# Kernel optimization log

Hardware: AMD Instinct MI355X
Metric: run time of the kernel (lower is better)

The kernel has to match this reference:

```python
import jax, jax.numpy as jnp
import numpy as np
from jax import lax

B, Hm, Wm = 8, 128, 128          # batch, mesh height, mesh width
DIM, HEADS, DH, G, K = 128, 8, 64, 64, 3
INNER = HEADS * DH
N = Hm * Wm


def setup_inputs() -> dict:
    key = jax.random.key(0)
    ks = jax.random.split(key, 12)
    s = 0.02
    x = jax.random.normal(ks[0], (B, N, DIM), dtype=jnp.float32)
    conv_fx_w = jax.random.normal(ks[1], (K, K, DIM, INNER), dtype=jnp.float32) * s
    conv_fx_b = jnp.zeros((INNER,), dtype=jnp.float32)
    conv_x_w = jax.random.normal(ks[2], (K, K, DIM, INNER), dtype=jnp.float32) * s
    conv_x_b = jnp.zeros((INNER,), dtype=jnp.float32)
    # nn.Linear(dim_head, slice_num): weight (G, DH), orthogonal-init approximated by scaled normal
    slice_w = jax.random.normal(ks[3], (G, DH), dtype=jnp.float32) * (1.0 / np.sqrt(DH))
    slice_b = jnp.zeros((G,), dtype=jnp.float32)
    temperature = jnp.ones((1, HEADS, 1, 1), dtype=jnp.float32) * 0.5
    wq = jax.random.normal(ks[4], (DH, DH), dtype=jnp.float32) * s
    wk = jax.random.normal(ks[5], (DH, DH), dtype=jnp.float32) * s
    wv = jax.random.normal(ks[6], (DH, DH), dtype=jnp.float32) * s
    out_w = jax.random.normal(ks[7], (DIM, INNER), dtype=jnp.float32) * s
    out_b = jnp.zeros((DIM,), dtype=jnp.float32)
    return {
        "x": x,
        "conv_fx_w": conv_fx_w, "conv_fx_b": conv_fx_b,
        "conv_x_w": conv_x_w, "conv_x_b": conv_x_b,
        "slice_w": slice_w, "slice_b": slice_b,
        "temperature": temperature,
        "wq": wq, "wk": wk, "wv": wv,
        "out_w": out_w, "out_b": out_b,
    }


def _conv(z, w, b):
    # z: (B, H, W, Cin); w: (K, K, Cin, Cout); SAME padding, stride 1
    return lax.conv_general_dilated(
        z, w, window_strides=(1, 1), padding="SAME",
        dimension_numbers=("NHWC", "HWIO", "NHWC")) + b


def reference(x, conv_fx_w, conv_fx_b, conv_x_w, conv_x_b,
              slice_w, slice_b, temperature, wq, wk, wv, out_w, out_b):
    b, n, c = x.shape
    xi = x.reshape(b, Hm, Wm, c)
    # (B,H,W,INNER) -> (B,N,heads,dh) -> (B,heads,N,dh)
    fx_mid = _conv(xi, conv_fx_w, conv_fx_b).reshape(b, n, HEADS, DH).transpose(0, 2, 1, 3)
    x_mid = _conv(xi, conv_x_w, conv_x_b).reshape(b, n, HEADS, DH).transpose(0, 2, 1, 3)

    temp = jnp.clip(temperature, 0.1, 5.0)  # (1,heads,1,1)
    logits = (jnp.einsum("bhnc,gc->bhng", x_mid, slice_w) + slice_b) / temp
    slice_weights = jax.nn.softmax(logits, axis=-1)         # (B,heads,N,G)

    slice_norm = slice_weights.sum(axis=2)                   # (B,heads,G)
    slice_token = jnp.einsum("bhnc,bhng->bhgc", fx_mid, slice_weights)
    slice_token = slice_token / (slice_norm + 1e-5)[..., None]

    q = jnp.einsum("bhgc,dc->bhgd", slice_token, wq)
    k = jnp.einsum("bhgc,dc->bhgd", slice_token, wk)
    v = jnp.einsum("bhgc,dc->bhgd", slice_token, wv)

    scale = DH ** (-0.5)
    attn = jax.nn.softmax(jnp.einsum("bhgd,bhkd->bhgk", q, k) * scale, axis=-1)
    out_slice = jnp.einsum("bhgk,bhkd->bhgd", attn, v)       # (B,heads,G,dh)

    out_x = jnp.einsum("bhgc,bhng->bhnc", out_slice, slice_weights)
    out_x = out_x.transpose(0, 2, 1, 3).reshape(b, n, INNER)
    return jnp.einsum("bnc,dc->bnd", out_x, out_w) + out_b
```

## Files before the change

### kernel.cpp

```cpp
#include <hip/hip_runtime.h>
#include <stdint.h>

#define BATCH 8
#define HEADS 8
#define HM 128
#define WM 128
#define NPIX (HM*WM)
#define DIMC 128
#define DH 64
#define GS 64
#define INNER 512
#define KTOT 1152
#define XT_LD 128
#define PT_LD 128

typedef unsigned short u16;
typedef short v8s __attribute__((ext_vector_type(8)));
typedef float v4f __attribute__((ext_vector_type(4)));

__device__ __forceinline__ u16 f2bf(float f) {
    unsigned x = __float_as_uint(f);
    return (u16)((x + 0x7fffu + ((x >> 16) & 1u)) >> 16);
}
__device__ __forceinline__ float bf2f(u16 u) { return __uint_as_float(((unsigned)u) << 16); }
__device__ __forceinline__ unsigned cvtpk(float lo, float hi) {
    unsigned r;
    asm("v_cvt_pk_bf16_f32 %0, %1, %2" : "=v"(r) : "v"(lo), "v"(hi));
    return r;
}

union BF8 { uint4 v; u16 s[8]; };

__global__ __launch_bounds__(256) void k_build_w(
    const float* __restrict__ wx, const float* __restrict__ wfx,
    const float* __restrict__ slw, const float* __restrict__ temp,
    u16* __restrict__ wcatT, u16* __restrict__ wfxT)
{
    __shared__ float sw_l[GS][DH + 1];
    __shared__ float wx_l[INNER];
    int row = blockIdx.x;
    int t = threadIdx.x;
    for (int i = t; i < GS * DH; i += 256) sw_l[i >> 6][i & 63] = slw[i];
    for (int i = t; i < INNER; i += 256) wx_l[i] = wx[(size_t)row * INNER + i];
    __syncthreads();
#pragma unroll
    for (int j = 0; j < 2; j++) {
        int co = j * 256 + t;
        int h = co >> 6, g = co & 63;
        float s = 0.f;
        for (int c = 0; c < DH; c++) s = fmaf(wx_l[h * 64 + c], sw_l[g][c], s);
        float tv = fminf(fmaxf(temp[h], 0.1f), 5.0f);
        wcatT[(size_t)co * KTOT + row] = f2bf(s / tv);
        wfxT[(size_t)co * KTOT + row] = f2bf(wfx[(size_t)row * INNER + co]);
    }
}

__global__ __launch_bounds__(512) void k_build_b(
    const float* __restrict__ bx, const float* __restrict__ slw,
    const float* __restrict__ slb, const float* __restrict__ temp,
    float* __restrict__ bcatL)
{
    int co = threadIdx.x;
    int h = co >> 6, g = co & 63;
    float s = slb[g];
    for (int c = 0; c < DH; c++) s = fmaf(bx[h * 64 + c], slw[g * 64 + c], s);
    float tv = fminf(fmaxf(temp[h], 0.1f), 5.0f);
    bcatL[co] = s / tv;
}

union SmemC {
    u16 X[130 * XT_LD];
    struct { u16 SwT[128][PT_LD]; u16 FxT[128][PT_LD]; } e;
};

__global__ __launch_bounds__(256) void k_conv2(
    const float* __restrict__ xin, const u16* __restrict__ wcatT,
    const u16* __restrict__ wfxT, const float* __restrict__ bcatL,
    const float* __restrict__ bfx, u16* __restrict__ swbT,
    float* __restrict__ straw, float* __restrict__ norm)
{
    __shared__ SmemC sm;
    int pt = blockIdx.x;
    int b = pt >> 7, y = pt & 127;
    int ct = blockIdx.y;
    int cob = ct << 7;
    int t = threadIdx.x;
    int lane = t & 63, wave = t >> 6;
    int wr = wave >> 1, wc = wave & 1;
    int l16 = lane & 15, lk = lane >> 4;

    v4f accL[4][4], accF[4][4];
#pragma unroll
    for (int i = 0; i < 4; i++)
#pragma unroll
        for (int j = 0; j < 4; j++) {
            accL[i][j] = v4f{0.f, 0.f, 0.f, 0.f};
            accF[i][j] = v4f{0.f, 0.f, 0.f, 0.f};
        }

    const u16* wlb[4]; const u16* wfb[4];
#pragma unroll
    for (int nj = 0; nj < 4; nj++) {
        size_t roff = (size_t)(cob + wc * 64 + nj * 16 + l16) * KTOT + lk * 8;
        wlb[nj] = wcatT + roff;
        wfb[nj] = wfxT + roff;
    }

    v8s bL[2][4], bF[2][4];
    {
#pragma unroll
        for (int nj = 0; nj < 4; nj++) {
            bL[0][nj] = *(const v8s*)(wlb[nj]);
            bF[0][nj] = *(const v8s*)(wfb[nj]);
        }
    }

    for (int ky = 0; ky < 3; ky++) {
        int yy = y + ky - 1;
        bool yok = (unsigned)yy < (unsigned)HM;
        const float* xrow = xin + ((size_t)b * NPIX + (size_t)yy * WM) * DIMC;
        if (ky) __syncthreads();
        for (int i = t; i < 2080; i += 256) {
            int row = i >> 4, k8 = i & 15;
            int px = row - 1;
            uint4 o;
            if (yok && (unsigned)px < (unsigned)WM) {
                const float4* p = (const float4*)(xrow + (size_t)px * DIMC + k8 * 8);
                float4 fa = p[0], fb = p[1];
                o = make_uint4(cvtpk(fa.x, fa.y), cvtpk(fa.z, fa.w),
                               cvtpk(fb.x, fb.y), cvtpk(fb.z, fb.w));
            } else {
                o = make_uint4(0u, 0u, 0u, 0u);
            }
            *(uint4*)(sm.X + row * XT_LD + ((k8 ^ (row & 7)) * 8)) = o;
        }
        __syncthreads();
#pragma unroll
        for (int cc = 0; cc < 12; cc++) {
            int g = ky * 12 + cc;
            if (g < 35) {
                int wo = ((g + 1) >> 2) * 128 + ((g + 1) & 3) * 32;
#pragma unroll
                for (int nj = 0; nj < 4; nj++) {
                    bL[(cc + 1) & 1][nj] = *(const v8s*)(wlb[nj] + wo);
                    bF[(cc + 1) & 1][nj] = *(const v8s*)(wfb[nj] + wo);
                }
            }
            int kx = cc >> 2, c4 = cc & 3;
            int xr7 = (l16 + kx) & 7;
            const u16* xb = sm.X + (wr * 64 + l16 + kx) * XT_LD;
            int xo = (((c4 * 4 + lk) ^ xr7) * 8);
            v8s av[4];
#pragma unroll
            for (int mi = 0; mi < 4; mi++)
                av[mi] = *(const v8s*)(xb + mi * 16 * XT_LD + xo);
#pragma unroll
            for (int mi = 0; mi < 4; mi++)
#pragma unroll
                for (int nj = 0; nj < 4; nj++) {
                    accL[mi][nj] = __builtin_amdgcn_mfma_f32_16x16x32_bf16(
                        av[mi], bL[cc & 1][nj], accL[mi][nj], 0, 0, 0);
                    accF[mi][nj] = __builtin_amdgcn_mfma_f32_16x16x32_bf16(
                        av[mi], bF[cc & 1][nj], accF[mi][nj], 0, 0, 0);
                }
        }
    }
    __syncthreads();

    float bbL[4], bbF[4];
#pragma unroll
    for (int nj = 0; nj < 4; nj++) {
        bbL[nj] = bcatL[cob + wc * 64 + nj * 16 + l16];
        bbF[nj] = bfx[cob + wc * 64 + nj * 16 + l16];
    }

#pragma unroll
    for (int mi = 0; mi < 4; mi++) {
#pragma unroll
        for (int q = 0; q < 4; q++) {
            float m = accL[mi][0][q] + bbL[0];
#pragma unroll
            for (int nj = 1; nj < 4; nj++) m = fmaxf(m, accL[mi][nj][q] + bbL[nj]);
            m = fmaxf(m, __shfl_xor(m, 1));
            m = fmaxf(m, __shfl_xor(m, 2));
            m = fmaxf(m, __shfl_xor(m, 4));
            m = fmaxf(m, __shfl_xor(m, 8));
            float ssum = 0.f;
#pragma unroll
            for (int nj = 0; nj < 4; nj++) {
                float e = __expf(accL[mi][nj][q] + bbL[nj] - m);
                accL[mi][nj][q] = e; ssum += e;
            }
            ssum += __shfl_xor(ssum, 1);
            ssum += __shfl_xor(ssum, 2);
            ssum += __shfl_xor(ssum, 4);
            ssum += __shfl_xor(ssum, 8);
            float inv = 1.f / ssum;
#pragma unroll
            for (int nj = 0; nj < 4; nj++) accL[mi][nj][q] *= inv;
        }
    }

#pragma unroll
    for (int nj = 0; nj < 4; nj++) {
        float pn = 0.f;
#pragma unroll
        for (int mi = 0; mi < 4; mi++)
#pragma unroll
            for (int q = 0; q < 4; q++) pn += accL[mi][nj][q];
        pn += __shfl_xor(pn, 16);
        pn += __shfl_xor(pn, 32);
        if (lk == 0)
            atomicAdd(&norm[(size_t)(b * HEADS + 2 * ct + wc) * GS + nj * 16 + l16], pn);
    }

#pragma unroll
    for (int nj = 0; nj < 4; nj++) {
        int grow = wc * 64 + nj * 16 + l16;
        int r7 = l16 & 7;
#pragma unroll
        for (int mi = 0; mi < 4; mi++) {
            int off = (((wr * 8 + mi * 2 + (lk >> 1)) ^ r7) * 8) + (lk & 1) * 4;
            uint2 wv;
            wv.x = cvtpk(accL[mi][nj][0], accL[mi][nj][1]);
            wv.y = cvtpk(accL[mi][nj][2], accL[mi][nj][3]);
            *(uint2*)&sm.e.SwT[grow][off] = wv;
            uint2 fv;
            fv.x = cvtpk(accF[mi][nj][0] + bbF[nj], accF[mi][nj][1] + bbF[nj]);
            fv.y = cvtpk(accF[mi][nj][2] + bbF[nj], accF[mi][nj][3] + bbF[nj]);
            *(uint2*)&sm.e.FxT[grow][off] = fv;
        }
    }
    __syncthreads();

    v4f pacc[2][4];
#pragma unroll
    for (int i = 0; i < 2; i++)
#pragma unroll
        for (int j = 0; j < 4; j++) pacc[i][j] = v4f{0.f, 0.f, 0.f, 0.f};
    {
        int r7 = l16 & 7;
#pragma unroll
        for (int c = 0; c < 4; c++) {
            int ko = (((c * 4 + lk) ^ r7) * 8);
            v8s aw[2], bw[4];
#pragma unroll
            for (int mi = 0; mi < 2; mi++)
                aw[mi] = *(const v8s*)(&sm.e.SwT[wc * 64 + wr * 32 + mi * 16 + l16][0] + ko);
#pragma unroll
            for (int nj = 0; nj < 4; nj++)
                bw[nj] = *(const v8s*)(&sm.e.FxT[wc * 64 + nj * 16 + l16][0] + ko);
#pragma unroll
            for (int mi = 0; mi < 2; mi++)
#pragma unroll
                for (int nj = 0; nj < 4; nj++)
                    pacc[mi][nj] = __builtin_amdgcn_mfma_f32_16x16x32_bf16(
                        aw[mi], bw[nj], pacc[mi][nj], 0, 0, 0);
        }
    }

#pragma unroll
    for (int it = 0; it < 8; it++) {
        int chunk = it * 256 + t;
        int g = chunk >> 4;
        int p8 = chunk & 15;
        uint4 v = *(const uint4*)(&sm.e.SwT[g][0] + ((p8 ^ (g & 7)) * 8));
        size_t di = (((size_t)(b * HEADS + 2 * ct + (g >> 6)) * GS + (g & 63)) * NPIX)
                    + (size_t)y * WM + p8 * 8;
        *(uint4*)&swbT[di] = v;
    }

    int bh = b * HEADS + 2 * ct + wc;
#pragma unroll
    for (int mi = 0; mi < 2; mi++)
#pragma unroll
        for (int nj = 0; nj < 4; nj++)
#pragma unroll
            for (int q = 0; q < 4; q++) {
                int g = wr * 32 + mi * 16 + lk * 4 + q;
                int dh = nj * 16 + l16;
                atomicAdd(&straw[((size_t)bh * GS + g) * DH + dh], pacc[mi][nj][q]);
            }
}

__global__ __launch_bounds__(256) void k_attn(
    const float* __restrict__ straw, const float* __restrict__ norm,
    const float* __restrict__ wq, const float* __restrict__ wk, const float* __restrict__ wv,
    const float* __restrict__ outw, float* __restrict__ m1)
{
    __shared__ float lds[4][64][64];
    int bh = blockIdx.x, h = bh & 7;
    int t = threadIdx.x;
    for (int i = t; i < 4096; i += 256) {
        int g = i >> 6;
        lds[0][g][i & 63] = straw[(size_t)bh * 4096 + i] / (norm[bh * 64 + g] + 1e-5f);
    }
    __syncthreads();
    int g = t >> 2, d0 = (t & 3) << 4;
    for (int d = d0; d < d0 + 16; d++) {
        float sq = 0.f, sk = 0.f, sv = 0.f;
        for (int c = 0; c < 64; c++) {
            float sc = lds[0][g][c];
            sq = fmaf(sc, wq[d * 64 + c], sq);
            sk = fmaf(sc, wk[d * 64 + c], sk);
            sv = fmaf(sc, wv[d * 64 + c], sv);
        }
        lds[1][g][d] = sq; lds[2][g][d] = sk; lds[3][g][d] = sv;
    }
    __syncthreads();
    float attnrow[16];
    for (int k2 = d0, i = 0; k2 < d0 + 16; k2++, i++) {
        float s = 0.f;
        for (int d = 0; d < 64; d++) s = fmaf(lds[1][g][d], lds[2][k2][d], s);
        attnrow[i] = s * 0.125f;
    }
    __syncthreads();
    for (int i = 0; i < 16; i++) lds[0][g][d0 + i] = attnrow[i];
    __syncthreads();
    if (t < 64) {
        float mx = -1e30f;
        for (int j = 0; j < 64; j++) mx = fmaxf(mx, lds[0][t][j]);
        float s = 0.f;
        for (int j = 0; j < 64; j++) { float e = __expf(lds[0][t][j] - mx); lds[0][t][j] = e; s += e; }
        float inv = 1.f / s;
        for (int j = 0; j < 64; j++) lds[0][t][j] *= inv;
    }
    __syncthreads();
    float osrow[16];
    for (int d = d0, i = 0; d < d0 + 16; d++, i++) {
        float s = 0.f;
        for (int kx = 0; kx < 64; kx++) s = fmaf(lds[0][g][kx], lds[3][kx][d], s);
        osrow[i] = s;
    }
    __syncthreads();
    for (int i = 0; i < 16; i++) lds[2][g][d0 + i] = osrow[i];
    __syncthreads();
    int dimb = (t & 3) << 5;
    for (int dim = dimb; dim < dimb + 32; dim++) {
        float s = 0.f;
        for (int c = 0; c < 64; c++)
            s = fmaf(lds[2][g][c], outw[(size_t)dim * INNER + h * 64 + c], s);
        m1[((size_t)bh * 64 + g) * DIMC + dim] = s;
    }
}

__global__ __launch_bounds__(256) void k_final(
    const u16* __restrict__ swbT, const float* __restrict__ m1,
    const float* __restrict__ outb, float* __restrict__ out)
{
    __shared__ float As[32][68];
    __shared__ float Bs[32][128];
    int b = blockIdx.x, nt = blockIdx.y;
    int t = threadIdx.x;
    int tn = t & 15, tm = t >> 4;
    float acc[4][8];
#pragma unroll
    for (int i = 0; i < 4; i++)
#pragma unroll
        for (int j = 0; j < 8; j++) acc[i][j] = 0.f;
    int n0 = nt * 64;
    int gg = t >> 3, nq = (t & 7) * 8;
    int g2 = t >> 3, dd = (t & 7) * 16;
    for (int h = 0; h < HEADS; h++) {
        const u16* swp = swbT + (size_t)(b * HEADS + h) * GS * NPIX;
        const float* m1p = m1 + (size_t)(b * HEADS + h) * GS * DIMC;
        for (int g0 = 0; g0 < 64; g0 += 32) {
            __syncthreads();
            BF8 av8; av8.v = *(const uint4*)&swp[(size_t)(g0 + gg) * NPIX + n0 + nq];
#pragma unroll
            for (int i = 0; i < 8; i++) As[gg][nq + i] = bf2f(av8.s[i]);
            const float* bp = m1p + (size_t)(g0 + g2) * DIMC + dd;
            *(float4*)&Bs[g2][dd + 0]  = *(const float4*)(bp + 0);
            *(float4*)&Bs[g2][dd + 4]  = *(const float4*)(bp + 4);
            *(float4*)&Bs[g2][dd + 8]  = *(const float4*)(bp + 8);
            *(float4*)&Bs[g2][dd + 12] = *(const float4*)(bp + 12);
            __syncthreads();
#pragma unroll
            for (int kk = 0; kk < 32; kk++) {
                float4 a = *(const float4*)&As[kk][tm * 4];
                float4 b0 = *(const float4*)&Bs[kk][tn * 4];
                float4 b1 = *(const float4*)&Bs[kk][tn * 4 + 64];
                float av[4] = {a.x, a.y, a.z, a.w};
                float bv[8] = {b0.x, b0.y, b0.z, b0.w, b1.x, b1.y, b1.z, b1.w};
#pragma unroll
                for (int i = 0; i < 4; i++)
#pragma unroll
                    for (int j = 0; j < 8; j++)
                        acc[i][j] = fmaf(av[i], bv[j], acc[i][j]);
            }
        }
    }
    float4 bias0 = *(const float4*)&outb[tn * 4];
    float4 bias1 = *(const float4*)&outb[64 + tn * 4];
#pragma unroll
    for (int i = 0; i < 4; i++) {
        size_t n = (size_t)n0 + tm * 4 + i;
        size_t rb = ((size_t)b * NPIX + n) * DIMC;
        float4 r0, r1;
        r0.x = acc[i][0] + bias0.x; r0.y = acc[i][1] + bias0.y;
        r0.z = acc[i][2] + bias0.z; r0.w = acc[i][3] + bias0.w;
        r1.x = acc[i][4] + bias1.x; r1.y = acc[i][5] + bias1.y;
        r1.z = acc[i][6] + bias1.z; r1.w = acc[i][7] + bias1.w;
        *(float4*)&out[rb + tn * 4] = r0;
        *(float4*)&out[rb + 64 + tn * 4] = r1;
    }
}

extern "C" void kernel_launch(void* const* d_in, const int* in_sizes, int n_in,
                              void* d_out, int out_size, void* d_ws, size_t ws_size,
                              hipStream_t stream)
{
    (void)in_sizes; (void)n_in; (void)out_size;
    const float* x    = (const float*)d_in[0];
    const float* wfx  = (const float*)d_in[1];
    const float* bfx  = (const float*)d_in[2];
    const float* wx   = (const float*)d_in[3];
    const float* bx   = (const float*)d_in[4];
    const float* slw  = (const float*)d_in[5];
    const float* slb  = (const float*)d_in[6];
    const float* temp = (const float*)d_in[7];
    const float* wq   = (const float*)d_in[8];
    const float* wk   = (const float*)d_in[9];
    const float* wv   = (const float*)d_in[10];
    const float* outw = (const float*)d_in[11];
    const float* outb = (const float*)d_in[12];
    float* out = (float*)d_out;
    float* W = (float*)d_ws;

    u16*   wcatT = (u16*)W;
    u16*   wfxT  = (u16*)(W + 294912);
    float* bcatL = W + 589824;
    float* norm  = W + 590336;
    float* straw = W + 594432;
    float* m1    = W + 856576;
    u16*   swbT  = (u16*)(W + 1380864);
    const size_t need = 1380864ull * 4 + 67108864ull * 2;
    if (ws_size < need) return;

    hipMemsetAsync(norm, 0, (4096 + 262144) * sizeof(float), stream);

    k_build_w<<<dim3(1152), 256, 0, stream>>>(wx, wfx, slw, temp, wcatT, wfxT);
    k_build_b<<<dim3(1), 512, 0, stream>>>(bx, slw, slb, temp, bcatL);
    k_conv2<<<dim3(1024, 4), 256, 0, stream>>>(x, wcatT, wfxT, bcatL, bfx, swbT, straw, norm);
    k_attn<<<dim3(64), 256, 0, stream>>>(straw, norm, wq, wk, wv, outw, m1);
    k_final<<<dim3(8, 256), 256, 0, stream>>>(swbT, m1, outb, out);
}
```

Before: 1.312 ms.

## Widen conv block to 256 output channels with 512 threads to reuse input tile

The fused conv kernel now computes 256 output channels (four heads) per block using 8 waves instead of 128 channels with 4 waves. The staged bf16 input row tile is loaded once per block, so half as many blocks each redo the fp32 load and conversion of the input rows. The epilogue (slice-token MFMA, swbT store, atomics) is processed in two head-pair passes through the same shared buffer, which adds extra barriers. The 512-thread blocks with large accumulator arrays may cut occupancy and raise register pressure.

```diff
diff --git a/kernel.cpp b/kernel.cpp
--- a/kernel.cpp
+++ b/kernel.cpp
@@ -73,7 +73,7 @@
     struct { u16 SwT[128][PT_LD]; u16 FxT[128][PT_LD]; } e;
 };
 
-__global__ __launch_bounds__(256) void k_conv2(
+__global__ __launch_bounds__(512) void k_conv2(
     const float* __restrict__ xin, const u16* __restrict__ wcatT,
     const u16* __restrict__ wfxT, const float* __restrict__ bcatL,
     const float* __restrict__ bfx, u16* __restrict__ swbT,
@@ -83,11 +83,12 @@
     int pt = blockIdx.x;
     int b = pt >> 7, y = pt & 127;
     int ct = blockIdx.y;
-    int cob = ct << 7;
+    int cob = ct << 8;
     int t = threadIdx.x;
     int lane = t & 63, wave = t >> 6;
-    int wr = wave >> 1, wc = wave & 1;
+    int w_half = wave >> 2, w_co = wave & 3;
     int l16 = lane & 15, lk = lane >> 4;
+    int hb = b * HEADS + 4 * ct;
 
     v4f accL[4][4], accF[4][4];
 #pragma unroll
@@ -101,38 +102,41 @@
     const u16* wlb[4]; const u16* wfb[4];
 #pragma unroll
     for (int nj = 0; nj < 4; nj++) {
-        size_t roff = (size_t)(cob + wc * 64 + nj * 16 + l16) * KTOT + lk * 8;
+        size_t roff = (size_t)(cob + w_co * 64 + nj * 16 + l16) * KTOT + lk * 8;
         wlb[nj] = wcatT + roff;
         wfb[nj] = wfxT + roff;
     }
 
     v8s bL[2][4], bF[2][4];
-    {
-#pragma unroll
-        for (int nj = 0; nj < 4; nj++) {
-            bL[0][nj] = *(const v8s*)(wlb[nj]);
-            bF[0][nj] = *(const v8s*)(wfb[nj]);
-        }
-    }
-
+#pragma unroll
+    for (int nj = 0; nj < 4; nj++) {
+        bL[0][nj] = *(const v8s*)(wlb[nj]);
+        bF[0][nj] = *(const v8s*)(wfb[nj]);
+    }
+
+#pragma unroll
     for (int ky = 0; ky < 3; ky++) {
         int yy = y + ky - 1;
         bool yok = (unsigned)yy < (unsigned)HM;
         const float* xrow = xin + ((size_t)b * NPIX + (size_t)yy * WM) * DIMC;
         if (ky) __syncthreads();
-        for (int i = t; i < 2080; i += 256) {
-            int row = i >> 4, k8 = i & 15;
-            int px = row - 1;
-            uint4 o;
-            if (yok && (unsigned)px < (unsigned)WM) {
-                const float4* p = (const float4*)(xrow + (size_t)px * DIMC + k8 * 8);
-                float4 fa = p[0], fb = p[1];
-                o = make_uint4(cvtpk(fa.x, fa.y), cvtpk(fa.z, fa.w),
-                               cvtpk(fb.x, fb.y), cvtpk(fb.z, fb.w));
-            } else {
-                o = make_uint4(0u, 0u, 0u, 0u);
-            }
-            *(uint4*)(sm.X + row * XT_LD + ((k8 ^ (row & 7)) * 8)) = o;
+#pragma unroll
+        for (int it = 0; it < 5; it++) {
+            int i = t + it * 512;
+            if (i < 2080) {
+                int row = i >> 4, k8 = i & 15;
+                int px = row - 1;
+                uint4 o;
+                if (yok && (unsigned)px < (unsigned)WM) {
+                    const float4* p = (const float4*)(xrow + (size_t)px * DIMC + k8 * 8);
+                    float4 fa = p[0], fb = p[1];
+                    o = make_uint4(cvtpk(fa.x, fa.y), cvtpk(fa.z, fa.w),
+                                   cvtpk(fb.x, fb.y), cvtpk(fb.z, fb.w));
+                } else {
+                    o = make_uint4(0u, 0u, 0u, 0u);
+                }
+                *(uint4*)(sm.X + row * XT_LD + ((k8 ^ (row & 7)) * 8)) = o;
+            }
         }
         __syncthreads();
 #pragma unroll
@@ -148,7 +152,7 @@
             }
             int kx = cc >> 2, c4 = cc & 3;
             int xr7 = (l16 + kx) & 7;
-            const u16* xb = sm.X + (wr * 64 + l16 + kx) * XT_LD;
+            const u16* xb = sm.X + (w_half * 64 + l16 + kx) * XT_LD;
             int xo = (((c4 * 4 + lk) ^ xr7) * 8);
             v8s av[4];
 #pragma unroll
@@ -170,8 +174,8 @@
     float bbL[4], bbF[4];
 #pragma unroll
     for (int nj = 0; nj < 4; nj++) {
-        bbL[nj] = bcatL[cob + wc * 64 + nj * 16 + l16];
-        bbF[nj] = bfx[cob + wc * 64 + nj * 16 + l16];
+        bbL[nj] = bcatL[cob + w_co * 64 + nj * 16 + l16];
+        bbF[nj] = bfx[cob + w_co * 64 + nj * 16 + l16];
     }
 
 #pragma unroll
@@ -211,76 +215,82 @@
         pn += __shfl_xor(pn, 16);
         pn += __shfl_xor(pn, 32);
         if (lk == 0)
-            atomicAdd(&norm[(size_t)(b * HEADS + 2 * ct + wc) * GS + nj * 16 + l16], pn);
-    }
-
-#pragma unroll
-    for (int nj = 0; nj < 4; nj++) {
-        int grow = wc * 64 + nj * 16 + l16;
-        int r7 = l16 & 7;
-#pragma unroll
-        for (int mi = 0; mi < 4; mi++) {
-            int off = (((wr * 8 + mi * 2 + (lk >> 1)) ^ r7) * 8) + (lk & 1) * 4;
-            uint2 wv;
-            wv.x = cvtpk(accL[mi][nj][0], accL[mi][nj][1]);
-            wv.y = cvtpk(accL[mi][nj][2], accL[mi][nj][3]);
-            *(uint2*)&sm.e.SwT[grow][off] = wv;
-            uint2 fv;
-            fv.x = cvtpk(accF[mi][nj][0] + bbF[nj], accF[mi][nj][1] + bbF[nj]);
-            fv.y = cvtpk(accF[mi][nj][2] + bbF[nj], accF[mi][nj][3] + bbF[nj]);
-            *(uint2*)&sm.e.FxT[grow][off] = fv;
-        }
-    }
-    __syncthreads();
-
-    v4f pacc[2][4];
-#pragma unroll
-    for (int i = 0; i < 2; i++)
-#pragma unroll
-        for (int j = 0; j < 4; j++) pacc[i][j] = v4f{0.f, 0.f, 0.f, 0.f};
-    {
-        int r7 = l16 & 7;
-#pragma unroll
-        for (int c = 0; c < 4; c++) {
-            int ko = (((c * 4 + lk) ^ r7) * 8);
-            v8s aw[2], bw[4];
+            atomicAdd(&norm[(size_t)(hb + w_co) * GS + nj * 16 + l16], pn);
+    }
+
+#pragma unroll
+    for (int hp = 0; hp < 2; hp++) {
+        bool mine = ((w_co >> 1) == hp);
+        if (mine) {
+            int wcp = w_co & 1;
+#pragma unroll
+            for (int nj = 0; nj < 4; nj++) {
+                int grow = wcp * 64 + nj * 16 + l16;
+                int r7 = l16 & 7;
+#pragma unroll
+                for (int mi = 0; mi < 4; mi++) {
+                    int off = (((w_half * 8 + mi * 2 + (lk >> 1)) ^ r7) * 8) + (lk & 1) * 4;
+                    uint2 wv;
+                    wv.x = cvtpk(accL[mi][nj][0], accL[mi][nj][1]);
+                    wv.y = cvtpk(accL[mi][nj][2], accL[mi][nj][3]);
+                    *(uint2*)&sm.e.SwT[grow][off] = wv;
+                    uint2 fv;
+                    fv.x = cvtpk(accF[mi][nj][0] + bbF[nj], accF[mi][nj][1] + bbF[nj]);
+                    fv.y = cvtpk(accF[mi][nj][2] + bbF[nj], accF[mi][nj][3] + bbF[nj]);
+                    *(uint2*)&sm.e.FxT[grow][off] = fv;
+                }
+            }
+        }
+        __syncthreads();
+        if (mine) {
+            int wcp = w_co & 1;
+            v4f pacc[2][4];
+#pragma unroll
+            for (int i = 0; i < 2; i++)
+#pragma unroll
+                for (int j = 0; j < 4; j++) pacc[i][j] = v4f{0.f, 0.f, 0.f, 0.f};
+            int r7 = l16 & 7;
+#pragma unroll
+            for (int c = 0; c < 4; c++) {
+                int ko = (((c * 4 + lk) ^ r7) * 8);
+                v8s aw[2], bw[4];
+#pragma unroll
+                for (int mi = 0; mi < 2; mi++)
+                    aw[mi] = *(const v8s*)(&sm.e.SwT[wcp * 64 + w_half * 32 + mi * 16 + l16][0] + ko);
+#pragma unroll
+                for (int nj = 0; nj < 4; nj++)
+                    bw[nj] = *(const v8s*)(&sm.e.FxT[wcp * 64 + nj * 16 + l16][0] + ko);
+#pragma unroll
+                for (int mi = 0; mi < 2; mi++)
+#pragma unroll
+                    for (int nj = 0; nj < 4; nj++)
+                        pacc[mi][nj] = __builtin_amdgcn_mfma_f32_16x16x32_bf16(
+                            aw[mi], bw[nj], pacc[mi][nj], 0, 0, 0);
+            }
+            int bh2 = hb + 2 * hp + wcp;
 #pragma unroll
             for (int mi = 0; mi < 2; mi++)
-                aw[mi] = *(const v8s*)(&sm.e.SwT[wc * 64 + wr * 32 + mi * 16 + l16][0] + ko);
-#pragma unroll
-            for (int nj = 0; nj < 4; nj++)
-                bw[nj] = *(const v8s*)(&sm.e.FxT[wc * 64 + nj * 16 + l16][0] + ko);
-#pragma unroll
-            for (int mi = 0; mi < 2; mi++)
 #pragma unroll
                 for (int nj = 0; nj < 4; nj++)
-                    pacc[mi][nj] = __builtin_amdgcn_mfma_f32_16x16x32_bf16(
-                        aw[mi], bw[nj], pacc[mi][nj], 0, 0, 0);
-        }
-    }
-
-#pragma unroll
-    for (int it = 0; it < 8; it++) {
-        int chunk = it * 256 + t;
-        int g = chunk >> 4;
-        int p8 = chunk & 15;
-        uint4 v = *(const uint4*)(&sm.e.SwT[g][0] + ((p8 ^ (g & 7)) * 8));
-        size_t di = (((size_t)(b * HEADS + 2 * ct + (g >> 6)) * GS + (g & 63)) * NPIX)
-                    + (size_t)y * WM + p8 * 8;
-        *(uint4*)&swbT[di] = v;
-    }
-
-    int bh = b * HEADS + 2 * ct + wc;
-#pragma unroll
-    for (int mi = 0; mi < 2; mi++)
-#pragma unroll
-        for (int nj = 0; nj < 4; nj++)
-#pragma unroll
-            for (int q = 0; q < 4; q++) {
-                int g = wr * 32 + mi * 16 + lk * 4 + q;
-                int dh = nj * 16 + l16;
-                atomicAdd(&straw[((size_t)bh * GS + g) * DH + dh], pacc[mi][nj][q]);
-            }
+#pragma unroll
+                    for (int q = 0; q < 4; q++) {
+                        int g = w_half * 32 + mi * 16 + lk * 4 + q;
+                        int dh = nj * 16 + l16;
+                        atomicAdd(&straw[((size_t)bh2 * GS + g) * DH + dh], pacc[mi][nj][q]);
+                    }
+        }
+#pragma unroll
+        for (int it = 0; it < 4; it++) {
+            int chunk = it * 512 + t;
+            int gi = chunk >> 4;
+            int p8 = chunk & 15;
+            uint4 v = *(const uint4*)(&sm.e.SwT[gi][0] + ((p8 ^ (gi & 7)) * 8));
+            size_t di = (((size_t)(hb + 2 * hp + (gi >> 6)) * GS + (gi & 63)) * NPIX)
+                        + (size_t)y * WM + p8 * 8;
+            *(uint4*)&swbT[di] = v;
+        }
+        __syncthreads();
+    }
 }
 
 __global__ __launch_bounds__(256) void k_attn(
@@ -441,7 +451,7 @@
 
     k_build_w<<<dim3(1152), 256, 0, stream>>>(wx, wfx, slw, temp, wcatT, wfxT);
     k_build_b<<<dim3(1), 512, 0, stream>>>(bx, slw, slb, temp, bcatL);
-    k_conv2<<<dim3(1024, 4), 256, 0, stream>>>(x, wcatT, wfxT, bcatL, bfx, swbT, straw, norm);
+    k_conv2<<<dim3(1024, 2), 512, 0, stream>>>(x, wcatT, wfxT, bcatL, bfx, swbT, straw, norm);
     k_attn<<<dim3(64), 256, 0, stream>>>(straw, norm, wq, wk, wv, outw, m1);
     k_final<<<dim3(8, 256), 256, 0, stream>>>(swbT, m1, outb, out);
 }
```

Result: faster. 1.192 ms (-9.2%).
